# Kernel tuning notes

Hardware: AMD Instinct MI355X
Metric: run time of the kernel (lower is better)

Reference implementation:

```python
import jax, jax.numpy as jnp
import numpy as np

HEADS = 8
DIM_HEAD = 64
SCALE = DIM_HEAD ** (-0.5)


def setup_inputs() -> dict:
    key = jax.random.key(0)
    k1, k2, k3 = jax.random.split(key, 3)
    b, l, c = 8, 4096, 512
    x = jax.random.normal(k1, (b, l, c), dtype=jnp.float32)
    w_qkv = jax.random.normal(k2, (3 * c, c), dtype=jnp.float32) * (c ** -0.5)
    w_out = jax.random.normal(k3, (c, c), dtype=jnp.float32) * (c ** -0.5)
    b_out = jnp.zeros((c,), dtype=jnp.float32)
    return {"x": x, "w_qkv": w_qkv, "w_out": w_out, "b_out": b_out}


def reference(x, w_qkv, w_out, b_out):
    b, l, c = x.shape
    h = HEADS
    lh = l // h
    # to_qkv: Linear(dim, 3*dim, bias=False)
    qkv = x @ w_qkv.T                                   # (b, l, 3c)
    qkv = qkv.reshape(b, lh, h, 3, c).transpose(3, 0, 2, 1, 4)  # (3, b, h, l/h, c)
    q, k, v = qkv[0], qkv[1], qkv[2]                    # each (b, h, l/h, c)
    # transpose(-2,-1): attention is over the CHANNEL axis
    q = jnp.swapaxes(q, -2, -1)                         # (b, h, c, l/h)
    k = jnp.swapaxes(k, -2, -1)                         # (b, h, c, l/h)
    v = jnp.swapaxes(v, -2, -1)                         # (b, h, c, l/h)
    attn = jnp.einsum('bhcl,bhdl->bhcd', q, k) * SCALE  # (b, h, c, c)
    attn = jax.nn.softmax(attn, axis=-1)
    y = jnp.einsum('bhcd,bhdl->bhcl', attn, v)          # (b, h, c, l/h)
    y = y.transpose(0, 3, 1, 2).reshape(b, l, c)        # (b, l/h, h, c) -> (b, l, c)
    # to_out: Linear(dim, dim) + Dropout (identity at eval)
    out = y @ w_out.T + b_out
    return out
```

## Files before the change

### kernel.cpp

```cpp
#include <hip/hip_runtime.h>
#include <stdint.h>
#include <stddef.h>

typedef _Float16 f16;
typedef _Float16 f16x8 __attribute__((ext_vector_type(8)));
typedef _Float16 f16x4 __attribute__((ext_vector_type(4)));
typedef float f32x4 __attribute__((ext_vector_type(4)));

__device__ __forceinline__ void gload16(const void* g, void* l) {
    auto gp = (const __attribute__((address_space(1))) uint32_t*)(uintptr_t)g;
    auto lp = (__attribute__((address_space(3))) uint32_t*)(uintptr_t)l;
    __builtin_amdgcn_global_load_lds(gp, lp, 16, 0, 0);
}

__device__ __forceinline__ f16x4 cvt4(f32x4 v) {
    return f16x4{ (f16)v[0], (f16)v[1], (f16)v[2], (f16)v[3] };
}

__global__ __launch_bounds__(256) void prep_k(const float* __restrict__ x,
                                              const float* __restrict__ wqkv,
                                              const float* __restrict__ wout,
                                              f16* __restrict__ xb,
                                              f16* __restrict__ wqb,
                                              f16* __restrict__ wob) {
    int tid = blockIdx.x * blockDim.x + threadIdx.x;
    int stride = gridDim.x * blockDim.x;
    for (int i = tid; i < 4194304; i += stride) {
        float4 v = ((const float4*)x)[i];
        *(f16x4*)(xb + (size_t)i * 4) = f16x4{ (f16)v.x, (f16)v.y, (f16)v.z, (f16)v.w };
    }
    for (int i = tid; i < 196608; i += stride) {
        float4 v = ((const float4*)wqkv)[i];
        *(f16x4*)(wqb + (size_t)i * 4) = f16x4{ (f16)v.x, (f16)v.y, (f16)v.z, (f16)v.w };
    }
    for (int i = tid; i < 65536; i += stride) {
        float4 v = ((const float4*)wout)[i];
        *(f16x4*)(wob + (size_t)i * 4) = f16x4{ (f16)v.x, (f16)v.y, (f16)v.z, (f16)v.w };
    }
}

#define W0  asm volatile("s_waitcnt vmcnt(0)" ::: "memory")
#define BAR __builtin_amdgcn_s_barrier()


#define A_STAGE(NB) do {                                                        \
    gload16(Ab + kb + sE,          &ldsA[NB][( 0 + wid*8)*64]);                 \
    gload16(Ab + kb + sO + 32768,  &ldsA[NB][(32 + wid*8)*64]);                 \
    gload16(Ab + kb + sE + 65536,  &ldsA[NB][(64 + wid*8)*64]);                 \
    gload16(Ab + kb + sO + 98304,  &ldsA[NB][(96 + wid*8)*64]);                 \
    gload16(Bb + kb + sE,          &ldsB[NB][( 0 + wid*8)*64]);                 \
    gload16(Bb + kb + sO + 32768,  &ldsB[NB][(32 + wid*8)*64]);                 \
    gload16(Bb + kb + sE + 65536,  &ldsB[NB][(64 + wid*8)*64]);                 \
    gload16(Bb + kb + sO + 98304,  &ldsB[NB][(96 + wid*8)*64]);                 \
    kb += 128;                                                                  \
} while (0)

#define A_RD(SET, BUF) do {                                                     \
    _Pragma("unroll") for (int mi = 0; mi < 4; ++mi)                            \
    _Pragma("unroll") for (int kk = 0; kk < 2; ++kk)                            \
        aF##SET[mi][kk] = *(const f16x8*)(&ldsA[BUF][0] + aoff[mi][kk]);        \
    _Pragma("unroll") for (int ni = 0; ni < 4; ++ni)                            \
    _Pragma("unroll") for (int kk = 0; kk < 2; ++kk)                            \
        bF##SET[ni][kk] = *(const f16x8*)(&ldsB[BUF][0] + boff[ni][kk]);        \
} while (0)

#define A_MM(SET, KK, ML, MH_) do {                                             \
    __builtin_amdgcn_s_setprio(1);                                              \
    if (qk) {                                                                   \
        _Pragma("unroll") for (int mi = ML; mi < MH_; ++mi)                     \
        _Pragma("unroll") for (int ni = 0; ni < 4; ++ni)                        \
            acc[mi][ni] = __builtin_amdgcn_mfma_f32_16x16x32_f16(               \
                aF##SET[mi][KK], bF##SET[ni][KK], acc[mi][ni], 0, 0, 0);        \
    } else {                                                                    \
        _Pragma("unroll") for (int mi = ML; mi < MH_; ++mi)                     \
        _Pragma("unroll") for (int ni = 0; ni < 4; ++ni)                        \
            acc[mi][ni] = __builtin_amdgcn_mfma_f32_16x16x32_f16(               \
                bF##SET[ni][KK], aF##SET[mi][KK], acc[mi][ni], 0, 0, 0);        \
    }                                                                           \
    __builtin_amdgcn_s_setprio(0);                                              \
} while (0)

#define A_MM3(SET)   do { A_MM(SET, 0, 0, 2); A_MM(SET, 0, 2, 4); A_MM(SET, 1, 0, 2); } while (0)
#define A_MMLAST(SET) A_MM(SET, 1, 2, 4)

#define A_TILE(CUR, NXT, NB, STG, FINAL) do {                                   \
    if (STG) A_STAGE(NB);                                                       \
    A_MM3(CUR);                                                                 \
    if (!FINAL) { W0; BAR; A_RD(NXT, NB); }                                     \
    A_MMLAST(CUR);                                                              \
} while (0)

__global__ __launch_bounds__(256, 2) void g15_k(const f16* __restrict__ A0,
                                                const f16* __restrict__ B0,
                                                f16* __restrict__ Qd,
                                                f16* __restrict__ Kd,
                                                f16* __restrict__ Vd) {
    __shared__ f16 ldsA[2][8192];
    __shared__ f16 ldsB[2][8192];

    const int tid = threadIdx.x;
    const int lane = tid & 63;
    const int wid = tid >> 6;
    const int wr = wid >> 1;
    const int wc = wid & 1;

    const int bid = blockIdx.x;
    const bool qk = bid < 2048;
    int tm, tn;
    if (qk) {
        int swz = (bid & 7) * 256 + (bid >> 3);
        tm = (swz >> 3) * 128; tn = (swz & 7) * 128;
    } else {
        int b2 = bid - 2048;
        int swz = (b2 & 7) * 128 + (b2 >> 3);
        tm = (swz >> 2) * 128; tn = (swz & 3) * 128 + 1024;
    }

    const char* Ab = (const char*)(A0 + (size_t)tm * 512);
    const char* Bb = (const char*)(B0 + (size_t)tn * 512);

    const int u = tid >> 3;
    const int colE = ((tid & 7) ^ ((u & 7) ^ (u >> 3))) * 16;
    const int sE = u * 1024 + colE;
    const int sO = sE ^ 64;
    int kb = 0;

    int aoff[4][2], boff[4][2];
#pragma unroll
    for (int mi = 0; mi < 4; ++mi) {
        int r = qk ? ((lane & 15) * 8 + wr * 4 + mi)
                   : (wr * 64 + mi * 16 + (lane & 15));
#pragma unroll
        for (int kk = 0; kk < 2; ++kk) {
            int c8 = (lane >> 4) + kk * 4;
            aoff[mi][kk] = r * 64 + (c8 ^ ((r & 7) ^ ((r >> 3) & 7))) * 8;
        }
    }
#pragma unroll
    for (int ni = 0; ni < 4; ++ni) {
        int r = wc * 64 + ni * 16 + (lane & 15);
#pragma unroll
        for (int kk = 0; kk < 2; ++kk) {
            int c8 = (lane >> 4) + kk * 4;
            boff[ni][kk] = r * 64 + (c8 ^ ((r & 7) ^ ((r >> 3) & 7))) * 8;
        }
    }

    f32x4 acc[4][4] = {};
    f16x8 aF0[4][2], bF0[4][2], aF1[4][2], bF1[4][2];

    A_STAGE(0);
    W0; BAR;
    A_RD(0, 0);

#pragma unroll 1
    for (int i = 0; i < 3; ++i) {
        A_TILE(0, 1, 1, true, false);
        A_TILE(1, 0, 0, true, false);
    }
    A_TILE(0, 1, 1, true, false);
    A_TILE(1, 1, 1, false, true);

    if (qk) {
        const int b = tm >> 12;
        const int lt = (tm & 4095) >> 3;
        f16* dst = (tn < 512) ? Qd : Kd;
        const int cb = (tn & 511) + wc * 64;
        const int lh0 = lt + (lane >> 4) * 4;
#pragma unroll
        for (int mi = 0; mi < 4; ++mi) {
            int h = wr * 4 + mi;
#pragma unroll
            for (int ni = 0; ni < 4; ++ni) {
                int c = cb + ni * 16 + (lane & 15);
                *(f16x4*)(dst + ((size_t)((b * 8 + h) * 512 + c)) * 512 + lh0) =
                    cvt4(acc[mi][ni]);
            }
        }
    } else {
        f16* dst = Vd;
#pragma unroll
        for (int mi = 0; mi < 4; ++mi) {
            int t = tm + wr * 64 + mi * 16 + (lane & 15);
            int b = t >> 12, l = t & 4095;
            int h = l & 7, lh = l >> 3;
#pragma unroll
            for (int ni = 0; ni < 4; ++ni) {
                int d0 = (tn - 1024) + wc * 64 + ni * 16 + (lane >> 4) * 4;
                *(f16x4*)(dst + ((size_t)((b * 8 + h) * 512 + lh)) * 512 + d0) =
                    cvt4(acc[mi][ni]);
            }
        }
    }
}

#define S_STAGE(B) do {                                                         \
    gload16(Qt + kb + soff,           &ldsQ[B][(  0 + wid*8)*64]);              \
    gload16(Qt + kb + soff + 65536,   &ldsQ[B][( 64 + wid*8)*64]);              \
    gload16(Kt + kb + soff,           &ldsK[B][(  0 + wid*8)*64]);              \
    gload16(Kt + kb + soff + 65536,   &ldsK[B][( 64 + wid*8)*64]);              \
    gload16(Kt + kb + soff + 131072,  &ldsK[B][(128 + wid*8)*64]);              \
    gload16(Kt + kb + soff + 196608,  &ldsK[B][(192 + wid*8)*64]);              \
    gload16(Kt + kb + soff + 262144,  &ldsK[B][(256 + wid*8)*64]);              \
    gload16(Kt + kb + soff + 327680,  &ldsK[B][(320 + wid*8)*64]);              \
    gload16(Kt + kb + soff + 393216,  &ldsK[B][(384 + wid*8)*64]);              \
    gload16(Kt + kb + soff + 458752,  &ldsK[B][(448 + wid*8)*64]);              \
    kb += 128;                                                                  \
} while (0)

#define S_RD(KK, B) do {                                                        \
    _Pragma("unroll") for (int ni = 0; ni < 4; ++ni)                            \
        bF[ni] = *(const f16x8*)(&ldsK[B][0] + boff[ni][KK]);                   \
    _Pragma("unroll") for (int mi = 0; mi < 8; ++mi)                            \
        aF[mi] = *(const f16x8*)(&ldsQ[B][0] + aoff[mi][KK]);                   \
} while (0)

#define S_MM do {                                                               \
    __builtin_amdgcn_s_setprio(1);                                              \
    _Pragma("unroll") for (int mi = 0; mi < 8; ++mi)                            \
    _Pragma("unroll") for (int ni = 0; ni < 4; ++ni)                            \
        acc[mi][ni] = __builtin_amdgcn_mfma_f32_16x16x32_f16(                   \
            aF[mi], bF[ni], acc[mi][ni], 0, 0, 0);                              \
    __builtin_amdgcn_s_setprio(0);                                              \
} while (0)

__global__ __launch_bounds__(512) void sfm_k(const f16* __restrict__ Qb,
                                             const f16* __restrict__ Kb,
                                             f16* __restrict__ Pb) {
    __shared__ f16 ldsQ[2][8192];
    __shared__ f16 ldsK[2][32768];

    const int tid = threadIdx.x;
    const int lane = tid & 63;
    const int wid = tid >> 6;
    const int g = lane >> 4;
    const int li = lane & 15;

    const int bid = blockIdx.x;
    const int swz = (bid & 7) * 32 + (bid >> 3);
    const int bh = swz >> 2, ct = swz & 3;

    const char* Qt = (const char*)(Qb + (size_t)bh * 262144 + (size_t)ct * 128 * 512);
    const char* Kt = (const char*)(Kb + (size_t)bh * 262144);

    const int soff = (tid >> 3) * 1024 +
                     ((((lane & 7) ^ (lane >> 3) ^ wid) & 7) * 16);
    int kb = 0;

    int aoff[8][2], boff[4][2];
#pragma unroll
    for (int mi = 0; mi < 8; ++mi) {
        int r = mi * 16 + li;
        int s3 = (r & 7) ^ ((r >> 3) & 7);
#pragma unroll
        for (int kk = 0; kk < 2; ++kk)
            aoff[mi][kk] = r * 64 + (((g + kk * 4) ^ s3)) * 8;
    }
#pragma unroll
    for (int ni = 0; ni < 4; ++ni) {
        int r = wid * 64 + ni * 16 + li;
        int s3 = (r & 7) ^ ((r >> 3) & 7);
#pragma unroll
        for (int kk = 0; kk < 2; ++kk)
            boff[ni][kk] = r * 64 + (((g + kk * 4) ^ s3)) * 8;
    }

    f32x4 acc[8][4] = {};
    f16x8 aF[8], bF[4];

    S_STAGE(0);
#pragma unroll 1
    for (int t = 0; t < 8; ++t) {
        const int cb = t & 1;
        if (t < 7) {
            S_STAGE(cb ^ 1);
            asm volatile("s_waitcnt vmcnt(10)" ::: "memory");
        } else {
            W0;
        }
        BAR;
        S_RD(0, cb);
        S_MM;
        S_RD(1, cb);
        S_MM;
        BAR;
    }

    float* red  = (float*)&ldsQ[0][0];
    float* redg = (float*)&ldsK[0][0];

#pragma unroll
    for (int mi = 0; mi < 8; ++mi)
#pragma unroll
        for (int ni = 0; ni < 4; ++ni) acc[mi][ni] *= 0.125f;

#pragma unroll
    for (int mi = 0; mi < 8; ++mi)
#pragma unroll
        for (int j = 0; j < 4; ++j) {
            float v = fmaxf(fmaxf(acc[mi][0][j], acc[mi][1][j]),
                            fmaxf(acc[mi][2][j], acc[mi][3][j]));
#pragma unroll
            for (int off = 1; off < 16; off <<= 1) v = fmaxf(v, __shfl_xor(v, off, 64));
            if (li == 0) red[wid * 128 + mi * 16 + g * 4 + j] = v;
        }
    BAR;
    if (tid < 128) {
        float m = red[tid];
#pragma unroll
        for (int w = 1; w < 8; ++w) m = fmaxf(m, red[w * 128 + tid]);
        redg[tid] = m;
    }
    BAR;

#pragma unroll
    for (int mi = 0; mi < 8; ++mi)
#pragma unroll
        for (int j = 0; j < 4; ++j) {
            float mg = redg[mi * 16 + g * 4 + j];
            float s = 0.f;
#pragma unroll
            for (int ni = 0; ni < 4; ++ni) {
                float e = __expf(acc[mi][ni][j] - mg);
                acc[mi][ni][j] = e;
                s += e;
            }
#pragma unroll
            for (int off = 1; off < 16; off <<= 1) s += __shfl_xor(s, off, 64);
            if (li == 0) red[wid * 128 + mi * 16 + g * 4 + j] = s;
        }
    BAR;
    if (tid < 128) {
        float s = red[tid];
#pragma unroll
        for (int w = 1; w < 8; ++w) s += red[w * 128 + tid];
        redg[tid] = 1.0f / s;
    }
    BAR;

    f16* Pt = Pb + (size_t)bh * 262144;
#pragma unroll
    for (int mi = 0; mi < 8; ++mi)
#pragma unroll
        for (int j = 0; j < 4; ++j) {
            int row = mi * 16 + g * 4 + j;
            float is = redg[row];
            size_t base = (size_t)(ct * 128 + row) * 512 + wid * 64 + li;
#pragma unroll
            for (int ni = 0; ni < 4; ++ni)
                Pt[base + ni * 16] = (f16)(acc[mi][ni][j] * is);
        }
}

#define B_STAGE(NB) do {                                                        \
    gload16(At + soff,          &ldsA2[NB][(  0 + wid*8)*64]);                  \
    gload16(At + soff + 65536,  &ldsA2[NB][( 64 + wid*8)*64]);                  \
    gload16(At + soff + 131072, &ldsA2[NB][(128 + wid*8)*64]);                  \
    gload16(At + soff + 196608, &ldsA2[NB][(192 + wid*8)*64]);                  \
    gload16(Bt + soff,          &ldsB2[NB][(  0 + wid*8)*64]);                  \
    gload16(Bt + soff + 65536,  &ldsB2[NB][( 64 + wid*8)*64]);                  \
    gload16(Bt + soff + 131072, &ldsB2[NB][(128 + wid*8)*64]);                  \
    gload16(Bt + soff + 196608, &ldsB2[NB][(192 + wid*8)*64]);                  \
    At += 128; Bt += 128;                                                       \
} while (0)

#define B_RD12(KK, BUF) do {                                                    \
    _Pragma("unroll") for (int ni = 0; ni < 4; ++ni)                            \
        bF[ni] = *(const f16x8*)(&ldsB2[BUF][0] + boff[ni][KK]);                \
    _Pragma("unroll") for (int mi = 0; mi < 8; ++mi)                            \
        aF[mi] = *(const f16x8*)(&ldsA2[BUF][0] + aoff[mi][KK]);                \
} while (0)

#define B_MM32 do {                                                             \
    __builtin_amdgcn_s_setprio(1);                                              \
    _Pragma("unroll") for (int mi = 0; mi < 8; ++mi)                            \
    _Pragma("unroll") for (int ni = 0; ni < 4; ++ni) {                          \
        if constexpr (SWP)                                                      \
            acc[mi][ni] = __builtin_amdgcn_mfma_f32_16x16x32_f16(               \
                bF[ni], aF[mi], acc[mi][ni], 0, 0, 0);                          \
        else                                                                    \
            acc[mi][ni] = __builtin_amdgcn_mfma_f32_16x16x32_f16(               \
                aF[mi], bF[ni], acc[mi][ni], 0, 0, 0);                          \
    }                                                                           \
    __builtin_amdgcn_s_setprio(0);                                              \
} while (0)

#define B_TILE(CB, NB, STG, FINAL) do {                                         \
    B_RD12(0, CB);                                                              \
    if (STG) B_STAGE(NB);                                                       \
    B_MM32;                                                                     \
    B_RD12(1, CB);                                                              \
    B_MM32;                                                                     \
    if (!FINAL) { W0; BAR; }                                                    \
} while (0)

template <int MODE, bool SWP>
__global__ __launch_bounds__(512) void g12_k(const f16* __restrict__ A0,
                                             const f16* __restrict__ B0,
                                             void* __restrict__ C0,
                                             const float* __restrict__ bias) {
    __shared__ f16 ldsA2[2][16384];
    __shared__ f16 ldsB2[2][16384];

    const int tid = threadIdx.x;
    const int lane = tid & 63;
    const int wid = tid >> 6;
    const int wr = wid >> 2;
    const int wc = wid & 3;

    const int bid = blockIdx.x;
    int tm, tn, bh = 0;
    if constexpr (MODE == 2) {
        int swz = (bid & 7) * 32 + (bid >> 3);
        bh = swz >> 2; tm = ((swz >> 1) & 1) * 256; tn = (swz & 1) * 256;
    } else {
        int swz = (bid & 7) * 32 + (bid >> 3);
        tm = (swz >> 1) * 256; tn = (swz & 1) * 256;
    }

    const size_t bhoff = (MODE == 2) ? (size_t)bh * 262144 : 0;
    const char* At = (const char*)(A0 + bhoff + (size_t)tm * 512);
    const char* Bt = (const char*)(B0 + bhoff + (size_t)tn * 512);

    const int soff = wid * 8192 + (lane >> 3) * 1024 +
                     ((((lane & 7) ^ (lane >> 3) ^ wid) & 7) * 16);

    int aoff[8][2], boff[4][2];
#pragma unroll
    for (int mi = 0; mi < 8; ++mi) {
        int r = wr * 128 + mi * 16 + (lane & 15);
        int s3 = (r & 7) ^ ((r >> 3) & 7);
#pragma unroll
        for (int kk = 0; kk < 2; ++kk)
            aoff[mi][kk] = r * 64 + ((((lane >> 4) + kk * 4) ^ s3)) * 8;
    }
#pragma unroll
    for (int ni = 0; ni < 4; ++ni) {
        int r = wc * 64 + ni * 16 + (lane & 15);
        int s3 = (r & 7) ^ ((r >> 3) & 7);
#pragma unroll
        for (int kk = 0; kk < 2; ++kk)
            boff[ni][kk] = r * 64 + ((((lane >> 4) + kk * 4) ^ s3)) * 8;
    }

    f32x4 acc[8][4] = {};
    f16x8 aF[8], bF[4];

    B_STAGE(0);
    W0; BAR;

#pragma unroll 1
    for (int i = 0; i < 3; ++i) {
        B_TILE(0, 1, true, false);
        B_TILE(1, 0, true, false);
    }
    B_TILE(0, 1, true, false);
    B_TILE(1, 1, false, true);

    if constexpr (MODE == 2) {
        f16* yb = (f16*)C0;
        const int b = bh >> 3, h = bh & 7;
#pragma unroll
        for (int mi = 0; mi < 8; ++mi) {
            int c0 = tm + wr * 128 + mi * 16 + (lane >> 4) * 4;
#pragma unroll
            for (int ni = 0; ni < 4; ++ni) {
                int l = tn + wc * 64 + ni * 16 + (lane & 15);
                size_t tok = (size_t)b * 4096 + (size_t)l * 8 + h;
                *(f16x4*)(yb + tok * 512 + c0) = cvt4(acc[mi][ni]);
            }
        }
    } else {
        float* O = (float*)C0;
#pragma unroll
        for (int mi = 0; mi < 8; ++mi) {
            int m = tm + wr * 128 + mi * 16 + (lane & 15);
#pragma unroll
            for (int ni = 0; ni < 4; ++ni) {
                int n0 = tn + wc * 64 + ni * 16 + (lane >> 4) * 4;
                float4 bv = *(const float4*)(bias + n0);
                f32x4 v = acc[mi][ni];
                v[0] += bv.x; v[1] += bv.y; v[2] += bv.z; v[3] += bv.w;
                *(f32x4*)(O + (size_t)m * 512 + n0) = v;
            }
        }
    }
}

extern "C" void kernel_launch(void* const* d_in, const int* in_sizes, int n_in,
                              void* d_out, int out_size, void* d_ws, size_t ws_size,
                              hipStream_t stream) {
    const float* x = (const float*)d_in[0];
    const float* wqkv = (const float*)d_in[1];
    const float* wout = (const float*)d_in[2];
    const float* bout = (const float*)d_in[3];
    float* out = (float*)d_out;
    char* ws = (char*)d_ws;
    const size_t MBs = 1u << 20;

    f16* xb  = (f16*)(ws + 0);
    f16* wqb = (f16*)(ws + 32 * MBs);
    f16* wob = (f16*)(ws + 34 * MBs);
    f16* Qb  = (f16*)(ws + 35 * MBs);
    f16* Kb  = (f16*)(ws + 67 * MBs);
    f16* Vb  = (f16*)(ws + 99 * MBs);
    f16* Pb  = xb;
    f16* yb  = Qb;

    prep_k<<<1024, 256, 0, stream>>>(x, wqkv, wout, xb, wqb, wob);
    g15_k<<<3072, 256, 0, stream>>>(xb, wqb, Qb, Kb, Vb);
    sfm_k<<<256, 512, 0, stream>>>(Qb, Kb, Pb);
    g12_k<2, false><<<256, 512, 0, stream>>>(Pb, Vb, yb, nullptr);
    g12_k<3, true><<<256, 512, 0, stream>>>(yb, wob, out, bout);
}
```

Measured before the change: 188.2 us.

## Fuse softmax and P·V into one attention kernel, keeping P in LDS

The softmax kernel no longer writes the normalized probability tile to global memory. It stores it swizzled into shared memory and then streams V tiles in, computing P·V in the same block, so the separate P·V GEMM launch is gone. This removes the global write and re-read of P (about 32 MB of fp16) and one kernel launch. In exchange the P·V loop is single-buffered with a full wait and barrier on every V tile, so its load latency is not overlapped, and only 256 blocks of 512 threads with a large LDS footprint run at once.

```diff
diff --git a/kernel.cpp b/kernel.cpp
--- a/kernel.cpp
+++ b/kernel.cpp
@@ -41,7 +41,6 @@
 
 #define W0  asm volatile("s_waitcnt vmcnt(0)" ::: "memory")
 #define BAR __builtin_amdgcn_s_barrier()
-
 
 #define A_STAGE(NB) do {                                                        \
     gload16(Ab + kb + sE,          &ldsA[NB][( 0 + wid*8)*64]);                 \
@@ -194,28 +193,29 @@
     }
 }
 
-#define S_STAGE(B) do {                                                         \
-    gload16(Qt + kb + soff,           &ldsQ[B][(  0 + wid*8)*64]);              \
-    gload16(Qt + kb + soff + 65536,   &ldsQ[B][( 64 + wid*8)*64]);              \
-    gload16(Kt + kb + soff,           &ldsK[B][(  0 + wid*8)*64]);              \
-    gload16(Kt + kb + soff + 65536,   &ldsK[B][( 64 + wid*8)*64]);              \
-    gload16(Kt + kb + soff + 131072,  &ldsK[B][(128 + wid*8)*64]);              \
-    gload16(Kt + kb + soff + 196608,  &ldsK[B][(192 + wid*8)*64]);              \
-    gload16(Kt + kb + soff + 262144,  &ldsK[B][(256 + wid*8)*64]);              \
-    gload16(Kt + kb + soff + 327680,  &ldsK[B][(320 + wid*8)*64]);              \
-    gload16(Kt + kb + soff + 393216,  &ldsK[B][(384 + wid*8)*64]);              \
-    gload16(Kt + kb + soff + 458752,  &ldsK[B][(448 + wid*8)*64]);              \
+
+#define F_STAGE(B) do {                                                         \
+    gload16(Qt + kb + soff,           &L[65536 + (B)*8192 + ( 0 + wid*8)*64]);  \
+    gload16(Qt + kb + soff + 65536,   &L[65536 + (B)*8192 + (64 + wid*8)*64]);  \
+    gload16(Kt + kb + soff,           &L[(B)*32768 + (  0 + wid*8)*64]);        \
+    gload16(Kt + kb + soff + 65536,   &L[(B)*32768 + ( 64 + wid*8)*64]);        \
+    gload16(Kt + kb + soff + 131072,  &L[(B)*32768 + (128 + wid*8)*64]);        \
+    gload16(Kt + kb + soff + 196608,  &L[(B)*32768 + (192 + wid*8)*64]);        \
+    gload16(Kt + kb + soff + 262144,  &L[(B)*32768 + (256 + wid*8)*64]);        \
+    gload16(Kt + kb + soff + 327680,  &L[(B)*32768 + (320 + wid*8)*64]);        \
+    gload16(Kt + kb + soff + 393216,  &L[(B)*32768 + (384 + wid*8)*64]);        \
+    gload16(Kt + kb + soff + 458752,  &L[(B)*32768 + (448 + wid*8)*64]);        \
     kb += 128;                                                                  \
 } while (0)
 
-#define S_RD(KK, B) do {                                                        \
+#define F_RD(KK, B) do {                                                        \
     _Pragma("unroll") for (int ni = 0; ni < 4; ++ni)                            \
-        bF[ni] = *(const f16x8*)(&ldsK[B][0] + boff[ni][KK]);                   \
+        bF[ni] = *(const f16x8*)(&L[(B)*32768] + boff[ni][KK]);                 \
     _Pragma("unroll") for (int mi = 0; mi < 8; ++mi)                            \
-        aF[mi] = *(const f16x8*)(&ldsQ[B][0] + aoff[mi][KK]);                   \
-} while (0)
-
-#define S_MM do {                                                               \
+        aF[mi] = *(const f16x8*)(&L[65536 + (B)*8192] + aoff[mi][KK]);          \
+} while (0)
+
+#define F_MM do {                                                               \
     __builtin_amdgcn_s_setprio(1);                                              \
     _Pragma("unroll") for (int mi = 0; mi < 8; ++mi)                            \
     _Pragma("unroll") for (int ni = 0; ni < 4; ++ni)                            \
@@ -224,11 +224,11 @@
     __builtin_amdgcn_s_setprio(0);                                              \
 } while (0)
 
-__global__ __launch_bounds__(512) void sfm_k(const f16* __restrict__ Qb,
-                                             const f16* __restrict__ Kb,
-                                             f16* __restrict__ Pb) {
-    __shared__ f16 ldsQ[2][8192];
-    __shared__ f16 ldsK[2][32768];
+__global__ __launch_bounds__(512) void attn_k(const f16* __restrict__ Qb,
+                                              const f16* __restrict__ Kb,
+                                              const f16* __restrict__ Vb,
+                                              f16* __restrict__ yb) {
+    __shared__ __align__(16) f16 L[81920];
 
     const int tid = threadIdx.x;
     const int lane = tid & 63;
@@ -239,9 +239,11 @@
     const int bid = blockIdx.x;
     const int swz = (bid & 7) * 32 + (bid >> 3);
     const int bh = swz >> 2, ct = swz & 3;
+    const int b = bh >> 3, h = bh & 7;
 
     const char* Qt = (const char*)(Qb + (size_t)bh * 262144 + (size_t)ct * 128 * 512);
     const char* Kt = (const char*)(Kb + (size_t)bh * 262144);
+    const char* Vt = (const char*)(Vb + (size_t)bh * 262144);
 
     const int soff = (tid >> 3) * 1024 +
                      ((((lane & 7) ^ (lane >> 3) ^ wid) & 7) * 16);
@@ -268,26 +270,26 @@
     f32x4 acc[8][4] = {};
     f16x8 aF[8], bF[4];
 
-    S_STAGE(0);
+    F_STAGE(0);
 #pragma unroll 1
     for (int t = 0; t < 8; ++t) {
         const int cb = t & 1;
         if (t < 7) {
-            S_STAGE(cb ^ 1);
+            F_STAGE(cb ^ 1);
             asm volatile("s_waitcnt vmcnt(10)" ::: "memory");
         } else {
             W0;
         }
         BAR;
-        S_RD(0, cb);
-        S_MM;
-        S_RD(1, cb);
-        S_MM;
+        F_RD(0, cb);
+        F_MM;
+        F_RD(1, cb);
+        F_MM;
         BAR;
     }
 
-    float* red  = (float*)&ldsQ[0][0];
-    float* redg = (float*)&ldsK[0][0];
+    float* red  = (float*)&L[65536];
+    float* redg = (float*)&L[65536 + 2048];
 
 #pragma unroll
     for (int mi = 0; mi < 8; ++mi)
@@ -338,18 +340,73 @@
     }
     BAR;
 
-    f16* Pt = Pb + (size_t)bh * 262144;
 #pragma unroll
     for (int mi = 0; mi < 8; ++mi)
 #pragma unroll
         for (int j = 0; j < 4; ++j) {
-            int row = mi * 16 + g * 4 + j;
-            float is = redg[row];
-            size_t base = (size_t)(ct * 128 + row) * 512 + wid * 64 + li;
+            int c = mi * 16 + g * 4 + j;
+            int s3c = (c & 7) ^ ((c >> 3) & 7);
+            float is = redg[c];
+#pragma unroll
+            for (int ni = 0; ni < 4; ++ni) {
+                int dch = wid * 8 + ni * 2 + (li >> 3);
+                L[c * 512 + ((dch ^ s3c) << 3) + (li & 7)] =
+                    (f16)(acc[mi][ni][j] * is);
+            }
+        }
+    BAR;
+
+#pragma unroll
+    for (int mi = 0; mi < 8; ++mi)
+#pragma unroll
+        for (int ni = 0; ni < 4; ++ni) acc[mi][ni] = f32x4{0.f, 0.f, 0.f, 0.f};
+
+    const int voff = (lane >> 2) * 1024 +
+                     ((((lane & 3) ^ ((lane >> 2) & 3) ^ g) & 3) * 16);
+
+#pragma unroll 1
+    for (int dt = 0; dt < 16; ++dt) {
+#pragma unroll
+        for (int i = 0; i < 4; ++i) {
+            int r0 = (wid * 4 + i) * 16;
+            gload16(Vt + (size_t)r0 * 1024 + dt * 64 + voff,
+                    &L[65536 + r0 * 32]);
+        }
+        W0; BAR;
+        f16x8 aP[8], bV[4];
+#pragma unroll
+        for (int mi = 0; mi < 8; ++mi) {
+            int c = mi * 16 + li;
+            int s3c = (c & 7) ^ ((c >> 3) & 7);
+            aP[mi] = *(const f16x8*)&L[c * 512 + (((dt * 4 + g) ^ s3c) << 3)];
+        }
+#pragma unroll
+        for (int ni = 0; ni < 4; ++ni) {
+            int lr = wid * 64 + ni * 16 + li;
+            int s2 = (lr & 3) ^ ((lr >> 2) & 3);
+            bV[ni] = *(const f16x8*)&L[65536 + lr * 32 + ((g ^ s2) & 3) * 8];
+        }
+        __builtin_amdgcn_s_setprio(1);
+#pragma unroll
+        for (int mi = 0; mi < 8; ++mi)
 #pragma unroll
             for (int ni = 0; ni < 4; ++ni)
-                Pt[base + ni * 16] = (f16)(acc[mi][ni][j] * is);
-        }
+                acc[mi][ni] = __builtin_amdgcn_mfma_f32_16x16x32_f16(
+                    aP[mi], bV[ni], acc[mi][ni], 0, 0, 0);
+        __builtin_amdgcn_s_setprio(0);
+        BAR;
+    }
+
+#pragma unroll
+    for (int mi = 0; mi < 8; ++mi) {
+        int c0 = ct * 128 + mi * 16 + g * 4;
+#pragma unroll
+        for (int ni = 0; ni < 4; ++ni) {
+            int l = wid * 64 + ni * 16 + li;
+            size_t tok = (size_t)b * 4096 + (size_t)l * 8 + h;
+            *(f16x4*)(yb + tok * 512 + c0) = cvt4(acc[mi][ni]);
+        }
+    }
 }
 
 #define B_STAGE(NB) do {                                                        \
@@ -374,14 +431,9 @@
 #define B_MM32 do {                                                             \
     __builtin_amdgcn_s_setprio(1);                                              \
     _Pragma("unroll") for (int mi = 0; mi < 8; ++mi)                            \
-    _Pragma("unroll") for (int ni = 0; ni < 4; ++ni) {                          \
-        if constexpr (SWP)                                                      \
-            acc[mi][ni] = __builtin_amdgcn_mfma_f32_16x16x32_f16(               \
-                bF[ni], aF[mi], acc[mi][ni], 0, 0, 0);                          \
-        else                                                                    \
-            acc[mi][ni] = __builtin_amdgcn_mfma_f32_16x16x32_f16(               \
-                aF[mi], bF[ni], acc[mi][ni], 0, 0, 0);                          \
-    }                                                                           \
+    _Pragma("unroll") for (int ni = 0; ni < 4; ++ni)                            \
+        acc[mi][ni] = __builtin_amdgcn_mfma_f32_16x16x32_f16(                   \
+            bF[ni], aF[mi], acc[mi][ni], 0, 0, 0);                              \
     __builtin_amdgcn_s_setprio(0);                                              \
 } while (0)
 
@@ -394,10 +446,9 @@
     if (!FINAL) { W0; BAR; }                                                    \
 } while (0)
 
-template <int MODE, bool SWP>
-__global__ __launch_bounds__(512) void g12_k(const f16* __restrict__ A0,
+__global__ __launch_bounds__(512) void out_k(const f16* __restrict__ A0,
                                              const f16* __restrict__ B0,
-                                             void* __restrict__ C0,
+                                             float* __restrict__ O,
                                              const float* __restrict__ bias) {
     __shared__ f16 ldsA2[2][16384];
     __shared__ f16 ldsB2[2][16384];
@@ -409,18 +460,11 @@
     const int wc = wid & 3;
 
     const int bid = blockIdx.x;
-    int tm, tn, bh = 0;
-    if constexpr (MODE == 2) {
-        int swz = (bid & 7) * 32 + (bid >> 3);
-        bh = swz >> 2; tm = ((swz >> 1) & 1) * 256; tn = (swz & 1) * 256;
-    } else {
-        int swz = (bid & 7) * 32 + (bid >> 3);
-        tm = (swz >> 1) * 256; tn = (swz & 1) * 256;
-    }
-
-    const size_t bhoff = (MODE == 2) ? (size_t)bh * 262144 : 0;
-    const char* At = (const char*)(A0 + bhoff + (size_t)tm * 512);
-    const char* Bt = (const char*)(B0 + bhoff + (size_t)tn * 512);
+    int swz = (bid & 7) * 32 + (bid >> 3);
+    int tm = (swz >> 1) * 256, tn = (swz & 1) * 256;
+
+    const char* At = (const char*)(A0 + (size_t)tm * 512);
+    const char* Bt = (const char*)(B0 + (size_t)tn * 512);
 
     const int soff = wid * 8192 + (lane >> 3) * 1024 +
                      ((((lane & 7) ^ (lane >> 3) ^ wid) & 7) * 16);
@@ -457,32 +501,16 @@
     B_TILE(0, 1, true, false);
     B_TILE(1, 1, false, true);
 
-    if constexpr (MODE == 2) {
-        f16* yb = (f16*)C0;
-        const int b = bh >> 3, h = bh & 7;
-#pragma unroll
-        for (int mi = 0; mi < 8; ++mi) {
-            int c0 = tm + wr * 128 + mi * 16 + (lane >> 4) * 4;
-#pragma unroll
-            for (int ni = 0; ni < 4; ++ni) {
-                int l = tn + wc * 64 + ni * 16 + (lane & 15);
-                size_t tok = (size_t)b * 4096 + (size_t)l * 8 + h;
-                *(f16x4*)(yb + tok * 512 + c0) = cvt4(acc[mi][ni]);
-            }
-        }
-    } else {
-        float* O = (float*)C0;
-#pragma unroll
-        for (int mi = 0; mi < 8; ++mi) {
-            int m = tm + wr * 128 + mi * 16 + (lane & 15);
-#pragma unroll
-            for (int ni = 0; ni < 4; ++ni) {
-                int n0 = tn + wc * 64 + ni * 16 + (lane >> 4) * 4;
-                float4 bv = *(const float4*)(bias + n0);
-                f32x4 v = acc[mi][ni];
-                v[0] += bv.x; v[1] += bv.y; v[2] += bv.z; v[3] += bv.w;
-                *(f32x4*)(O + (size_t)m * 512 + n0) = v;
-            }
+#pragma unroll
+    for (int mi = 0; mi < 8; ++mi) {
+        int m = tm + wr * 128 + mi * 16 + (lane & 15);
+#pragma unroll
+        for (int ni = 0; ni < 4; ++ni) {
+            int n0 = tn + wc * 64 + ni * 16 + (lane >> 4) * 4;
+            float4 bv = *(const float4*)(bias + n0);
+            f32x4 v = acc[mi][ni];
+            v[0] += bv.x; v[1] += bv.y; v[2] += bv.z; v[3] += bv.w;
+            *(f32x4*)(O + (size_t)m * 512 + n0) = v;
         }
     }
 }
@@ -504,12 +532,10 @@
     f16* Qb  = (f16*)(ws + 35 * MBs);
     f16* Kb  = (f16*)(ws + 67 * MBs);
     f16* Vb  = (f16*)(ws + 99 * MBs);
-    f16* Pb  = xb;
-    f16* yb  = Qb;
+    f16* yb  = xb;
 
     prep_k<<<1024, 256, 0, stream>>>(x, wqkv, wout, xb, wqb, wob);
     g15_k<<<3072, 256, 0, stream>>>(xb, wqb, Qb, Kb, Vb);
-    sfm_k<<<256, 512, 0, stream>>>(Qb, Kb, Pb);
-    g12_k<2, false><<<256, 512, 0, stream>>>(Pb, Vb, yb, nullptr);
-    g12_k<3, true><<<256, 512, 0, stream>>>(yb, wob, out, bout);
-}
+    attn_k<<<256, 512, 0, stream>>>(Qb, Kb, Vb, yb);
+    out_k<<<256, 512, 0, stream>>>(yb, wob, out, bout);
+}
```

New measurement: 188.7 us. Within noise of the previous version (+0.3%).
